# Performance work log

Hardware: AMD Instinct MI355X
Metric: run time of the kernel (lower is better)

## Reference

```python
import math
import jax, jax.numpy as jnp
import numpy as np


def setup_inputs() -> dict:
    key = jax.random.key(0)
    k1, k2 = jax.random.split(key)
    B, Sq, Sk, H, Hkv, D = 2, 2048, 2048, 16, 8, 128
    q = jax.random.normal(k1, (B, Sq, H, D), dtype=jnp.float32)
    kv = jax.random.normal(k2, (B, Sk, 2, Hkv, D), dtype=jnp.float32)
    return {"q": q, "kv": kv}


def reference(q, kv):
    # q: [B, Sq, H, D]; kv: [B, Sk, 2, Hkv, D]
    B, Sq, H, D = q.shape
    Sk = kv.shape[1]
    Hkv = kv.shape[3]
    if Hkv != H:
        # GQA: repeat each kv head g times consecutively ('... hkv d -> ... (hkv g) d')
        kv = jnp.repeat(kv, H // Hkv, axis=3)
    k = kv[:, :, 0]  # [B, Sk, H, D]
    v = kv[:, :, 1]  # [B, Sk, H, D]
    q = q.astype(jnp.float32)
    k = k.astype(jnp.float32)
    scale = 1.0 / math.sqrt(D)
    # scores: [B, H, Sq, Sk]
    scores = jnp.einsum('bqhd,bkhd->bhqk', q, k * scale)
    # causal mask with right-alignment offset: mask where col > row + Sk - Sq
    rows = jnp.arange(Sq)[:, None]
    cols = jnp.arange(Sk)[None, :]
    causal_mask = cols > rows + (Sk - Sq)  # [Sq, Sk]
    scores = jnp.where(causal_mask[None, None], jnp.float32(-10000.0), scores)
    attention = jax.nn.softmax(scores, axis=-1).astype(v.dtype)
    # output: [B, Sq, H, D]
    out = jnp.einsum('bhqk,bkhd->bqhd', attention, v)
    return out
```

## Files before the change

kernel.cpp:

```cpp
#include <hip/hip_runtime.h>
#include <stdint.h>


#define SQ 2048
#define SK 2048
#define NH 16
#define NKV 8
#define DH 128
#define KVSTRIDE (2*NKV*DH)
#define SCALE_LOG2E 0.12751743f

typedef __attribute__((ext_vector_type(8))) short bf8;
typedef __attribute__((ext_vector_type(4))) short v4s;
typedef __attribute__((ext_vector_type(4))) float f4;

#if __has_builtin(__builtin_amdgcn_mfma_f32_16x16x16bf16_1k)
#define HAVE_MFMA_K16 1
#else
#define HAVE_MFMA_K16 0
#endif

__device__ __forceinline__ float fast_exp2(float x) {
  return __builtin_amdgcn_exp2f(x);
}

__device__ __forceinline__ short f2bf(float f) {
  uint32_t u = __builtin_bit_cast(uint32_t, f);
  u += 0x7FFFu + ((u >> 16) & 1u);
  return (short)(u >> 16);
}

__device__ __forceinline__ bf8 pack8(f4 a, f4 b) {
  bf8 v;
  v[0] = f2bf(a[0]); v[1] = f2bf(a[1]); v[2] = f2bf(a[2]); v[3] = f2bf(a[3]);
  v[4] = f2bf(b[0]); v[5] = f2bf(b[1]); v[6] = f2bf(b[2]); v[7] = f2bf(b[3]);
  return v;
}
__device__ __forceinline__ bf8 pack8s(f4 a, f4 b, float s) {
  bf8 v;
  v[0] = f2bf(a[0]*s); v[1] = f2bf(a[1]*s); v[2] = f2bf(a[2]*s); v[3] = f2bf(a[3]*s);
  v[4] = f2bf(b[0]*s); v[5] = f2bf(b[1]*s); v[6] = f2bf(b[2]*s); v[7] = f2bf(b[3]*s);
  return v;
}

template<int CTRL>
__device__ __forceinline__ float dppmov(float x) {
  int xi = __builtin_bit_cast(int, x);
  int r = __builtin_amdgcn_update_dpp(xi, xi, CTRL, 0xF, 0xF, false);
  return __builtin_bit_cast(float, r);
}
__device__ __forceinline__ float rowsum16(float v) {
  v += dppmov<0x121>(v);
  v += dppmov<0x122>(v);
  v += dppmov<0x124>(v);
  v += dppmov<0x128>(v);
  return v;
}
__device__ __forceinline__ float rowmax16(float v) {
  v = fmaxf(v, dppmov<0x121>(v));
  v = fmaxf(v, dppmov<0x122>(v));
  v = fmaxf(v, dppmov<0x124>(v));
  v = fmaxf(v, dppmov<0x128>(v));
  return v;
}

__device__ __forceinline__ void g2l16(const short* g, short* l) {
  __builtin_amdgcn_global_load_lds(
      (const __attribute__((address_space(1))) uint32_t*)g,
      (__attribute__((address_space(3))) uint32_t*)l, 16, 0, 0);
}

__global__ void conv_kv(const float* __restrict__ kv,
                        short* __restrict__ Kb, short* __restrict__ Vb) {
  int id = blockIdx.x * 256 + threadIdx.x;
  if (blockIdx.y == 0) {
    int c   = id & 15;
    int key = (id >> 4) & 63;
    int kt  = (id >> 10) & 31;
    int hk  = (id >> 15) & 7;
    int b   = (id >> 18) & 1;
    const float* src = kv + ((size_t)(b * SK + kt * 64 + key) * 2) * (NKV * DH)
                          + hk * DH + c * 8;
    f4 a = *(const f4*)src;
    f4 bb = *(const f4*)(src + 4);
    short* dst = Kb + ((size_t)((b * 8 + hk) * 32 + kt)) * 8192;
    *(bf8*)&dst[(key * 16 + (c ^ (key & 7))) * 8] = pack8(a, bb);
  } else {
    int d  = id & 127;
    int c  = (id >> 7) & 7;
    int kt = (id >> 10) & 31;
    int hk = (id >> 15) & 7;
    int b  = (id >> 18) & 1;
    const float* src = kv + ((size_t)(b * SK + kt * 64 + c * 8) * 2 + 1) * (NKV * DH)
                          + hk * DH + d;
    bf8 v;
#pragma unroll
    for (int kk = 0; kk < 8; ++kk) v[kk] = f2bf(src[(size_t)kk * KVSTRIDE]);
    short* dst = Vb + ((size_t)((b * 8 + hk) * 32 + kt)) * 8192;
    *(bf8*)&dst[(d * 8 + (c ^ (d & 7))) * 8] = v;
  }
}

__launch_bounds__(512, 2)
__global__ void fa_fwd5(const float* __restrict__ q,
                        const short* __restrict__ Kb,
                        const short* __restrict__ Vb,
                        float* __restrict__ out) {
  __shared__ __align__(16) short heap[4][8192];

  const int tid  = threadIdx.x;
  const int w    = tid >> 6;
  const int l    = tid & 63;
  const int l15  = l & 15;
  const int quad = l >> 4;

  const int bx   = blockIdx.x;
  const int p    = bx >> 4;
  const int bhk  = bx & 15;
  const int b    = bhk >> 3;
  const int hk   = bhk & 7;
  const int side = w >> 2;
  const int w2   = w & 3;
  const int head  = hk * 2 + (w2 >> 1);
  const int rbase = (w2 & 1) * 32;
  const int myqt  = side ? (31 - p) : p;
  const int kmax  = 31 - p;
  const int q0    = myqt * 64;

  const short* ktiles = Kb + ((size_t)((b * 8 + hk) * 32)) * 8192;
  const short* vtiles = Vb + ((size_t)((b * 8 + hk) * 32)) * 8192;

  bf8 qf[2][4];
#pragma unroll
  for (int mt = 0; mt < 2; ++mt) {
    int row = q0 + rbase + mt * 16 + l15;
    const float* qr = q + ((size_t)(b * SQ + row) * NH + head) * DH;
#pragma unroll
    for (int kc = 0; kc < 4; ++kc) {
      const float* src = qr + kc * 32 + quad * 8;
      f4 a = *(const f4*)src;
      f4 c = *(const f4*)(src + 4);
      qf[mt][kc] = pack8s(a, c, SCALE_LOG2E);
    }
  }

  f4 O[2][8];
#pragma unroll
  for (int mt = 0; mt < 2; ++mt)
#pragma unroll
    for (int dt = 0; dt < 8; ++dt) O[mt][dt] = (f4){0.f, 0.f, 0.f, 0.f};
  float lpart[2] = {0.f, 0.f};

  auto stage = [&](int kt, int nb) {
    const short* ks = ktiles + (size_t)kt * 8192 + tid * 8;
    const short* vs = vtiles + (size_t)kt * 8192 + tid * 8;
    g2l16(ks,        &heap[nb][tid * 8]);
    g2l16(ks + 4096, &heap[nb][4096 + tid * 8]);
    g2l16(vs,        &heap[2 + nb][tid * 8]);
    g2l16(vs + 4096, &heap[2 + nb][4096 + tid * 8]);
  };

  stage(0, 0);

  for (int kt = 0; kt <= kmax; ++kt) {
    const int cur = kt & 1;
    __syncthreads();
    if (kt < kmax) stage(kt + 1, cur ^ 1);

    if (kt <= myqt) {
      const short* lk = heap[cur];
      const short* lv = heap[2 + cur];

      f4 S[2][4];
#pragma unroll
      for (int mt = 0; mt < 2; ++mt)
#pragma unroll
        for (int nt = 0; nt < 4; ++nt) S[mt][nt] = (f4){0.f, 0.f, 0.f, 0.f};
#pragma unroll
      for (int kc = 0; kc < 4; ++kc) {
#pragma unroll
        for (int nt = 0; nt < 4; ++nt) {
          int key = nt * 16 + l15;
          int c   = kc * 4 + quad;
          bf8 kf = *(const bf8*)&lk[(key * 16 + (c ^ (key & 7))) * 8];
          S[0][nt] = __builtin_amdgcn_mfma_f32_16x16x32_bf16(kf, qf[0][kc], S[0][nt], 0, 0, 0);
          S[1][nt] = __builtin_amdgcn_mfma_f32_16x16x32_bf16(kf, qf[1][kc], S[1][nt], 0, 0, 0);
        }
      }

      if (kt == myqt) {
#pragma unroll
        for (int nt = 0; nt < 4; ++nt)
#pragma unroll
          for (int r = 0; r < 4; ++r) {
            int keyl = nt * 16 + quad * 4 + r;
            if (keyl > rbase + l15)      S[0][nt][r] = -1e30f;
            if (keyl > rbase + 16 + l15) S[1][nt][r] = -1e30f;
          }
      }

      v4s pf[2][4];
#pragma unroll
      for (int mt = 0; mt < 2; ++mt)
#pragma unroll
        for (int nt = 0; nt < 4; ++nt) {
          f4 e;
#pragma unroll
          for (int r = 0; r < 4; ++r) {
            e[r] = fast_exp2(S[mt][nt][r]);
            lpart[mt] += e[r];
          }
          v4s pk;
          pk[0] = f2bf(e[0]); pk[1] = f2bf(e[1]);
          pk[2] = f2bf(e[2]); pk[3] = f2bf(e[3]);
          pf[mt][nt] = pk;
        }

#pragma unroll
      for (int kt16 = 0; kt16 < 4; ++kt16) {
#if !HAVE_MFMA_K16
        bf8 p0z = (bf8){pf[0][kt16][0], pf[0][kt16][1], pf[0][kt16][2], pf[0][kt16][3], 0, 0, 0, 0};
        bf8 p1z = (bf8){pf[1][kt16][0], pf[1][kt16][1], pf[1][kt16][2], pf[1][kt16][3], 0, 0, 0, 0};
#endif
#pragma unroll
        for (int dt = 0; dt < 8; ++dt) {
          int d = dt * 16 + l15;
          int c = kt16 * 2 + (quad >> 1);
          const short* vp = &lv[(d * 8 + (c ^ (d & 7))) * 8 + (quad & 1) * 4];
          v4s vf = *(const v4s*)vp;
#if HAVE_MFMA_K16
          O[0][dt] = __builtin_amdgcn_mfma_f32_16x16x16bf16_1k(vf, pf[0][kt16], O[0][dt], 0, 0, 0);
          O[1][dt] = __builtin_amdgcn_mfma_f32_16x16x16bf16_1k(vf, pf[1][kt16], O[1][dt], 0, 0, 0);
#else
          bf8 vz = (bf8){vf[0], vf[1], vf[2], vf[3], 0, 0, 0, 0};
          O[0][dt] = __builtin_amdgcn_mfma_f32_16x16x32_bf16(vz, p0z, O[0][dt], 0, 0, 0);
          O[1][dt] = __builtin_amdgcn_mfma_f32_16x16x32_bf16(vz, p1z, O[1][dt], 0, 0, 0);
#endif
        }
      }
    }
  }

#pragma unroll
  for (int mt = 0; mt < 2; ++mt) {
    float lsum = lpart[mt];
    lsum += __shfl_xor(lsum, 16, 64);
    lsum += __shfl_xor(lsum, 32, 64);
    float linv = 1.0f / lsum;
    int row = q0 + rbase + mt * 16 + l15;
    float* dst = out + ((size_t)(b * SQ + row) * NH + head) * DH + quad * 4;
#pragma unroll
    for (int dt = 0; dt < 8; ++dt) {
      f4 v;
      v[0] = O[mt][dt][0] * linv; v[1] = O[mt][dt][1] * linv;
      v[2] = O[mt][dt][2] * linv; v[3] = O[mt][dt][3] * linv;
      *(f4*)&dst[dt * 16] = v;
    }
  }
}

__launch_bounds__(256, 2)
__global__ void fa_fwd_v1(const float* __restrict__ q,
                          const float* __restrict__ kv,
                          float* __restrict__ out) {
  __shared__ __align__(16) short lsK[64 * 128];
  __shared__ __align__(16) short lsV[128 * 64];
  __shared__ __align__(16) short lsP[4][32 * 64];

  const int tid  = threadIdx.x;
  const int w    = tid >> 6;
  const int l    = tid & 63;
  const int l15  = l & 15;
  const int quad = l >> 4;

  const int bx  = blockIdx.x;
  const int qt  = 31 - (bx >> 4);
  const int bhk = bx & 15;
  const int b   = bhk >> 3;
  const int hk  = bhk & 7;
  const int head  = hk * 2 + (w >> 1);
  const int mrow0 = (w & 1) * 32;
  const int q0    = qt * 64;

  const float* kbase = kv + (size_t)b * SK * KVSTRIDE + (size_t)hk * DH;
  const float* vbase = kbase + NKV * DH;

  bf8 qf[2][4];
#pragma unroll
  for (int mt = 0; mt < 2; ++mt)
#pragma unroll
    for (int kc = 0; kc < 4; ++kc) {
      int row = q0 + mrow0 + mt * 16 + l15;
      int d0  = kc * 32 + quad * 8;
      const float* src = q + ((size_t)(b * SQ + row) * NH + head) * DH + d0;
      f4 a = *(const f4*)src;
      f4 c = *(const f4*)(src + 4);
      qf[mt][kc] = pack8s(a, c, SCALE_LOG2E);
    }

  f4 O[2][8];
  float mrow[2][4], lrow[2][4];
#pragma unroll
  for (int mt = 0; mt < 2; ++mt) {
#pragma unroll
    for (int nt = 0; nt < 8; ++nt) O[mt][nt] = (f4){0.f, 0.f, 0.f, 0.f};
#pragma unroll
    for (int r = 0; r < 4; ++r) { mrow[mt][r] = -1e30f; lrow[mt][r] = 0.f; }
  }

  for (int kt = 0; kt <= qt; ++kt) {
    if (kt) __syncthreads();
    const int k0 = kt * 64;
#pragma unroll
    for (int i = 0; i < 4; ++i) {
      int id  = i * 256 + tid;
      int key = id >> 4;
      int c   = id & 15;
      const float* src = kbase + (size_t)(k0 + key) * KVSTRIDE + c * 8;
      f4 a = *(const f4*)src;
      f4 bb = *(const f4*)(src + 4);
      *(bf8*)&lsK[(key * 16 + (c ^ (key & 7))) * 8] = pack8(a, bb);
    }
#pragma unroll
    for (int i = 0; i < 4; ++i) {
      int u  = i * 4 + w;
      int kg = u >> 1;
      int d  = (u & 1) * 64 + l;
      const float* src = vbase + (size_t)(k0 + kg * 8) * KVSTRIDE + d;
      bf8 v;
#pragma unroll
      for (int kk = 0; kk < 8; ++kk) v[kk] = f2bf(src[(size_t)kk * KVSTRIDE]);
      *(bf8*)&lsV[(d * 8 + (kg ^ (d & 7))) * 8] = v;
    }
    __syncthreads();

    f4 S[2][4];
#pragma unroll
    for (int mt = 0; mt < 2; ++mt)
#pragma unroll
      for (int nt = 0; nt < 4; ++nt) S[mt][nt] = (f4){0.f, 0.f, 0.f, 0.f};
#pragma unroll
    for (int kc = 0; kc < 4; ++kc)
#pragma unroll
      for (int nt = 0; nt < 4; ++nt) {
        int key = nt * 16 + l15;
        int c   = kc * 4 + quad;
        bf8 kf = *(const bf8*)&lsK[(key * 16 + (c ^ (key & 7))) * 8];
        S[0][nt] = __builtin_amdgcn_mfma_f32_16x16x32_bf16(qf[0][kc], kf, S[0][nt], 0, 0, 0);
        S[1][nt] = __builtin_amdgcn_mfma_f32_16x16x32_bf16(qf[1][kc], kf, S[1][nt], 0, 0, 0);
      }

    if (kt == qt) {
#pragma unroll
      for (int mt = 0; mt < 2; ++mt)
#pragma unroll
        for (int nt = 0; nt < 4; ++nt)
#pragma unroll
          for (int r = 0; r < 4; ++r) {
            int rloc = mrow0 + mt * 16 + quad * 4 + r;
            int kloc = nt * 16 + l15;
            if (kloc > rloc) S[mt][nt][r] = -1e30f;
          }
    }

#pragma unroll
    for (int mt = 0; mt < 2; ++mt)
#pragma unroll
      for (int r = 0; r < 4; ++r) {
        float mx = fmaxf(fmaxf(S[mt][0][r], S[mt][1][r]),
                         fmaxf(S[mt][2][r], S[mt][3][r]));
        mx = rowmax16(mx);
        float mold = mrow[mt][r];
        float mnew = fmaxf(mold, mx);
        float alpha = fast_exp2(mold - mnew);
        mrow[mt][r] = mnew;
        float rs = 0.f;
#pragma unroll
        for (int nt = 0; nt < 4; ++nt) {
          float pe = fast_exp2(S[mt][nt][r] - mnew);
          S[mt][nt][r] = pe;
          rs += pe;
        }
        rs = rowsum16(rs);
        lrow[mt][r] = lrow[mt][r] * alpha + rs;
#pragma unroll
        for (int nt = 0; nt < 8; ++nt) O[mt][nt][r] *= alpha;
        int m = mt * 16 + quad * 4 + r;
#pragma unroll
        for (int nt = 0; nt < 4; ++nt) {
          int key = nt * 16 + l15;
          lsP[w][(m * 8 + ((key >> 3) ^ (m & 7))) * 8 + (key & 7)] =
              f2bf(S[mt][nt][r]);
        }
      }

#pragma unroll
    for (int kc = 0; kc < 2; ++kc) {
      bf8 pf[2];
#pragma unroll
      for (int mt = 0; mt < 2; ++mt) {
        int m = mt * 16 + l15;
        int c = kc * 4 + quad;
        pf[mt] = *(const bf8*)&lsP[w][(m * 8 + (c ^ (m & 7))) * 8];
      }
#pragma unroll
      for (int nt = 0; nt < 8; ++nt) {
        int d = nt * 16 + l15;
        int c = kc * 4 + quad;
        bf8 vf = *(const bf8*)&lsV[(d * 8 + (c ^ (d & 7))) * 8];
        O[0][nt] = __builtin_amdgcn_mfma_f32_16x16x32_bf16(pf[0], vf, O[0][nt], 0, 0, 0);
        O[1][nt] = __builtin_amdgcn_mfma_f32_16x16x32_bf16(pf[1], vf, O[1][nt], 0, 0, 0);
      }
    }
  }

#pragma unroll
  for (int mt = 0; mt < 2; ++mt)
#pragma unroll
    for (int r = 0; r < 4; ++r) {
      float linv = 1.0f / lrow[mt][r];
      int row = q0 + mrow0 + mt * 16 + quad * 4 + r;
      float* dst = out + ((size_t)(b * SQ + row) * NH + head) * DH + l15;
#pragma unroll
      for (int nt = 0; nt < 8; ++nt) dst[nt * 16] = O[mt][nt][r] * linv;
    }
}

extern "C" void kernel_launch(void* const* d_in, const int* in_sizes, int n_in,
                              void* d_out, int out_size, void* d_ws, size_t ws_size,
                              hipStream_t stream) {
  const float* q  = (const float*)d_in[0];
  const float* kv = (const float*)d_in[1];
  float* out      = (float*)d_out;
  (void)in_sizes; (void)n_in; (void)out_size;

  const size_t kb_elems = (size_t)2 * 8 * 32 * 8192;
  const size_t need = 2 * kb_elems * sizeof(short);

  if (ws_size >= need) {
    short* Kb = (short*)d_ws;
    short* Vb = Kb + kb_elems;
    conv_kv<<<dim3(2048, 2), 256, 0, stream>>>(kv, Kb, Vb);
    fa_fwd5<<<dim3(256), dim3(512), 24576, stream>>>(q, Kb, Vb, out);
  } else {
    fa_fwd_v1<<<dim3(512), dim3(256), 0, stream>>>(q, kv, out);
  }
}
```

Before: 161.4 us.

## Split paired-tile blocks into one-tile blocks and re-swizzle V layout

Replaces the 512-thread blocks, which each handled a mirrored pair of query tiles (p and 31-p) for causal load balancing, with 256-thread blocks that each process a single query tile. Blocks are launched heaviest-first so the scheduler can balance the causal work. The V workspace layout is changed to a per-d row with an XOR swizzle over 4-element units, so the PV step can always use the 16x16x16 MFMA with conflict-free LDS reads. Row sums are accumulated as vectors. This trades explicit pairing for more, smaller blocks that rely on hardware scheduling to hide the imbalance, and each block now stages the full K/V tile with half as many threads.

```diff
diff --git a/kernel.cpp b/kernel.cpp
--- a/kernel.cpp
+++ b/kernel.cpp
@@ -13,12 +13,6 @@
 typedef __attribute__((ext_vector_type(8))) short bf8;
 typedef __attribute__((ext_vector_type(4))) short v4s;
 typedef __attribute__((ext_vector_type(4))) float f4;
-
-#if __has_builtin(__builtin_amdgcn_mfma_f32_16x16x16bf16_1k)
-#define HAVE_MFMA_K16 1
-#else
-#define HAVE_MFMA_K16 0
-#endif
 
 __device__ __forceinline__ float fast_exp2(float x) {
   return __builtin_amdgcn_exp2f(x);
@@ -86,23 +80,28 @@
     short* dst = Kb + ((size_t)((b * 8 + hk) * 32 + kt)) * 8192;
     *(bf8*)&dst[(key * 16 + (c ^ (key & 7))) * 8] = pack8(a, bb);
   } else {
-    int d  = id & 127;
-    int c  = (id >> 7) & 7;
+    int c3 = id & 7;
+    int d  = (id >> 3) & 127;
     int kt = (id >> 10) & 31;
     int hk = (id >> 15) & 7;
     int b  = (id >> 18) & 1;
-    const float* src = kv + ((size_t)(b * SK + kt * 64 + c * 8) * 2 + 1) * (NKV * DH)
-                          + hk * DH + d;
+    const float* vsrc = kv + ((size_t)(b * SK + kt * 64) * 2 + 1) * (NKV * DH)
+                           + hk * DH + d;
     bf8 v;
 #pragma unroll
-    for (int kk = 0; kk < 8; ++kk) v[kk] = f2bf(src[(size_t)kk * KVSTRIDE]);
+    for (int s = 0; s < 8; ++s) {
+      int unitp = c3 * 2 + (s >> 2);
+      int unit  = unitp ^ (d & 15);
+      int key   = (unit & 3) * 16 + (unit >> 2) * 4 + (s & 3);
+      v[s] = f2bf(vsrc[(size_t)key * KVSTRIDE]);
+    }
     short* dst = Vb + ((size_t)((b * 8 + hk) * 32 + kt)) * 8192;
-    *(bf8*)&dst[(d * 8 + (c ^ (d & 7))) * 8] = v;
-  }
-}
-
-__launch_bounds__(512, 2)
-__global__ void fa_fwd5(const float* __restrict__ q,
+    *(bf8*)&dst[d * 64 + c3 * 8] = v;
+  }
+}
+
+__launch_bounds__(256, 2)
+__global__ void fa_fwd6(const float* __restrict__ q,
                         const short* __restrict__ Kb,
                         const short* __restrict__ Vb,
                         float* __restrict__ out) {
@@ -114,18 +113,14 @@
   const int l15  = l & 15;
   const int quad = l >> 4;
 
-  const int bx   = blockIdx.x;
-  const int p    = bx >> 4;
-  const int bhk  = bx & 15;
-  const int b    = bhk >> 3;
-  const int hk   = bhk & 7;
-  const int side = w >> 2;
-  const int w2   = w & 3;
-  const int head  = hk * 2 + (w2 >> 1);
-  const int rbase = (w2 & 1) * 32;
-  const int myqt  = side ? (31 - p) : p;
-  const int kmax  = 31 - p;
-  const int q0    = myqt * 64;
+  const int bx  = blockIdx.x;
+  const int qt  = 31 - (bx >> 4);
+  const int bhk = bx & 15;
+  const int b   = bhk >> 3;
+  const int hk  = bhk & 7;
+  const int head  = hk * 2 + (w >> 1);
+  const int rbase = (w & 1) * 32;
+  const int q0    = qt * 64;
 
   const short* ktiles = Kb + ((size_t)((b * 8 + hk) * 32)) * 8192;
   const short* vtiles = Vb + ((size_t)((b * 8 + hk) * 32)) * 8192;
@@ -149,101 +144,87 @@
   for (int mt = 0; mt < 2; ++mt)
 #pragma unroll
     for (int dt = 0; dt < 8; ++dt) O[mt][dt] = (f4){0.f, 0.f, 0.f, 0.f};
-  float lpart[2] = {0.f, 0.f};
+  f4 lsum4[2] = {(f4){0.f,0.f,0.f,0.f}, (f4){0.f,0.f,0.f,0.f}};
 
   auto stage = [&](int kt, int nb) {
     const short* ks = ktiles + (size_t)kt * 8192 + tid * 8;
     const short* vs = vtiles + (size_t)kt * 8192 + tid * 8;
-    g2l16(ks,        &heap[nb][tid * 8]);
-    g2l16(ks + 4096, &heap[nb][4096 + tid * 8]);
-    g2l16(vs,        &heap[2 + nb][tid * 8]);
-    g2l16(vs + 4096, &heap[2 + nb][4096 + tid * 8]);
+#pragma unroll
+    for (int i = 0; i < 4; ++i) {
+      g2l16(ks + i * 2048, &heap[nb][i * 2048 + tid * 8]);
+      g2l16(vs + i * 2048, &heap[2 + nb][i * 2048 + tid * 8]);
+    }
   };
 
   stage(0, 0);
 
-  for (int kt = 0; kt <= kmax; ++kt) {
+  for (int kt = 0; kt <= qt; ++kt) {
     const int cur = kt & 1;
     __syncthreads();
-    if (kt < kmax) stage(kt + 1, cur ^ 1);
-
-    if (kt <= myqt) {
-      const short* lk = heap[cur];
-      const short* lv = heap[2 + cur];
-
-      f4 S[2][4];
-#pragma unroll
-      for (int mt = 0; mt < 2; ++mt)
-#pragma unroll
-        for (int nt = 0; nt < 4; ++nt) S[mt][nt] = (f4){0.f, 0.f, 0.f, 0.f};
-#pragma unroll
-      for (int kc = 0; kc < 4; ++kc) {
-#pragma unroll
-        for (int nt = 0; nt < 4; ++nt) {
-          int key = nt * 16 + l15;
-          int c   = kc * 4 + quad;
-          bf8 kf = *(const bf8*)&lk[(key * 16 + (c ^ (key & 7))) * 8];
-          S[0][nt] = __builtin_amdgcn_mfma_f32_16x16x32_bf16(kf, qf[0][kc], S[0][nt], 0, 0, 0);
-          S[1][nt] = __builtin_amdgcn_mfma_f32_16x16x32_bf16(kf, qf[1][kc], S[1][nt], 0, 0, 0);
+    if (kt < qt) stage(kt + 1, cur ^ 1);
+
+    const short* lk = heap[cur];
+    const short* lv = heap[2 + cur];
+
+    f4 S[2][4];
+#pragma unroll
+    for (int mt = 0; mt < 2; ++mt)
+#pragma unroll
+      for (int nt = 0; nt < 4; ++nt) S[mt][nt] = (f4){0.f, 0.f, 0.f, 0.f};
+#pragma unroll
+    for (int kc = 0; kc < 4; ++kc) {
+#pragma unroll
+      for (int nt = 0; nt < 4; ++nt) {
+        int key = nt * 16 + l15;
+        int c   = kc * 4 + quad;
+        bf8 kf = *(const bf8*)&lk[(key * 16 + (c ^ (key & 7))) * 8];
+        S[0][nt] = __builtin_amdgcn_mfma_f32_16x16x32_bf16(kf, qf[0][kc], S[0][nt], 0, 0, 0);
+        S[1][nt] = __builtin_amdgcn_mfma_f32_16x16x32_bf16(kf, qf[1][kc], S[1][nt], 0, 0, 0);
+      }
+    }
+
+    if (kt == qt) {
+#pragma unroll
+      for (int nt = 0; nt < 4; ++nt)
+#pragma unroll
+        for (int r = 0; r < 4; ++r) {
+          int keyl = nt * 16 + quad * 4 + r;
+          if (keyl > rbase + l15)      S[0][nt][r] = -1e30f;
+          if (keyl > rbase + 16 + l15) S[1][nt][r] = -1e30f;
         }
-      }
-
-      if (kt == myqt) {
-#pragma unroll
-        for (int nt = 0; nt < 4; ++nt)
-#pragma unroll
-          for (int r = 0; r < 4; ++r) {
-            int keyl = nt * 16 + quad * 4 + r;
-            if (keyl > rbase + l15)      S[0][nt][r] = -1e30f;
-            if (keyl > rbase + 16 + l15) S[1][nt][r] = -1e30f;
-          }
-      }
-
-      v4s pf[2][4];
-#pragma unroll
-      for (int mt = 0; mt < 2; ++mt)
-#pragma unroll
-        for (int nt = 0; nt < 4; ++nt) {
-          f4 e;
-#pragma unroll
-          for (int r = 0; r < 4; ++r) {
-            e[r] = fast_exp2(S[mt][nt][r]);
-            lpart[mt] += e[r];
-          }
-          v4s pk;
-          pk[0] = f2bf(e[0]); pk[1] = f2bf(e[1]);
-          pk[2] = f2bf(e[2]); pk[3] = f2bf(e[3]);
-          pf[mt][nt] = pk;
-        }
-
-#pragma unroll
-      for (int kt16 = 0; kt16 < 4; ++kt16) {
-#if !HAVE_MFMA_K16
-        bf8 p0z = (bf8){pf[0][kt16][0], pf[0][kt16][1], pf[0][kt16][2], pf[0][kt16][3], 0, 0, 0, 0};
-        bf8 p1z = (bf8){pf[1][kt16][0], pf[1][kt16][1], pf[1][kt16][2], pf[1][kt16][3], 0, 0, 0, 0};
-#endif
-#pragma unroll
-        for (int dt = 0; dt < 8; ++dt) {
-          int d = dt * 16 + l15;
-          int c = kt16 * 2 + (quad >> 1);
-          const short* vp = &lv[(d * 8 + (c ^ (d & 7))) * 8 + (quad & 1) * 4];
-          v4s vf = *(const v4s*)vp;
-#if HAVE_MFMA_K16
-          O[0][dt] = __builtin_amdgcn_mfma_f32_16x16x16bf16_1k(vf, pf[0][kt16], O[0][dt], 0, 0, 0);
-          O[1][dt] = __builtin_amdgcn_mfma_f32_16x16x16bf16_1k(vf, pf[1][kt16], O[1][dt], 0, 0, 0);
-#else
-          bf8 vz = (bf8){vf[0], vf[1], vf[2], vf[3], 0, 0, 0, 0};
-          O[0][dt] = __builtin_amdgcn_mfma_f32_16x16x32_bf16(vz, p0z, O[0][dt], 0, 0, 0);
-          O[1][dt] = __builtin_amdgcn_mfma_f32_16x16x32_bf16(vz, p1z, O[1][dt], 0, 0, 0);
-#endif
-        }
+    }
+
+    v4s pf[2][4];
+#pragma unroll
+    for (int mt = 0; mt < 2; ++mt)
+#pragma unroll
+      for (int nt = 0; nt < 4; ++nt) {
+        f4 e;
+#pragma unroll
+        for (int r = 0; r < 4; ++r) e[r] = fast_exp2(S[mt][nt][r]);
+        lsum4[mt] += e;
+        v4s pk;
+        pk[0] = f2bf(e[0]); pk[1] = f2bf(e[1]);
+        pk[2] = f2bf(e[2]); pk[3] = f2bf(e[3]);
+        pf[mt][nt] = pk;
+      }
+
+#pragma unroll
+    for (int t = 0; t < 4; ++t) {
+#pragma unroll
+      for (int dt = 0; dt < 8; ++dt) {
+        int d = dt * 16 + l15;
+        const short* vp = &lv[d * 64 + (((quad << 2) + t) ^ l15) * 4];
+        v4s vf = *(const v4s*)vp;
+        O[0][dt] = __builtin_amdgcn_mfma_f32_16x16x16bf16_1k(vf, pf[0][t], O[0][dt], 0, 0, 0);
+        O[1][dt] = __builtin_amdgcn_mfma_f32_16x16x16bf16_1k(vf, pf[1][t], O[1][dt], 0, 0, 0);
       }
     }
   }
 
 #pragma unroll
   for (int mt = 0; mt < 2; ++mt) {
-    float lsum = lpart[mt];
+    float lsum = lsum4[mt][0] + lsum4[mt][1] + lsum4[mt][2] + lsum4[mt][3];
     lsum += __shfl_xor(lsum, 16, 64);
     lsum += __shfl_xor(lsum, 32, 64);
     float linv = 1.0f / lsum;
@@ -441,7 +422,7 @@
     short* Kb = (short*)d_ws;
     short* Vb = Kb + kb_elems;
     conv_kv<<<dim3(2048, 2), 256, 0, stream>>>(kv, Kb, Vb);
-    fa_fwd5<<<dim3(256), dim3(512), 24576, stream>>>(q, Kb, Vb, out);
+    fa_fwd6<<<dim3(512), dim3(256), 0, stream>>>(q, Kb, Vb, out);
   } else {
     fa_fwd_v1<<<dim3(512), dim3(256), 0, stream>>>(q, kv, out);
   }
```

Result: no change. 158.8 us (-1.6%).
